# Kernel tuning notes

Measured on AMD Instinct MI355X. Metric: run time of the kernel, lower is better.

The kernel has to match this reference:

```python
import jax, jax.numpy as jnp
import numpy as np


def setup_inputs() -> dict:
    key = jax.random.key(0)
    ks = jax.random.split(key, 7)
    N, C, sy, sx = 1024, 384, 7, 7
    Dm, Dc = 64, 64
    Dg = C + Dm + Dc  # 512, must match f_t_global
    return {
        "f_t_global": jax.random.normal(ks[0], (N, Dg), dtype=jnp.float32),
        "x_t_local": jax.random.normal(ks[1], (N, C, sy, sx), dtype=jnp.float32),
        "x_t_prev_local": jax.random.normal(ks[2], (N, C, sy, sx), dtype=jnp.float32),
        "m_t": jax.random.normal(ks[3], (N, Dm), dtype=jnp.float32),
        "m_t_prev": jax.random.normal(ks[4], (N, Dm), dtype=jnp.float32),
        "c_t": jax.random.normal(ks[5], (N, Dc), dtype=jnp.float32),
        "c_t_prev": jax.random.normal(ks[6], (N, Dc), dtype=jnp.float32),
    }


def _join(loc, m, c):
    # loc: [S, N, C]; m: [N, Dm]; c: [N, Dc] -> [S, N, C+Dm+Dc]
    S, N, _ = loc.shape
    mc = jnp.concatenate([m, c], axis=-1)  # [N, Dm+Dc]
    mc = jnp.broadcast_to(mc[None], (S, N, mc.shape[-1]))
    return jnp.concatenate([loc, mc], axis=-1)


def _mean_ce_diag(logits):
    # logits: [S, N, N]; labels = arange(N) for every s -> mean over s of CE
    logp = jax.nn.log_softmax(logits, axis=-1)
    diag = jnp.diagonal(logp, axis1=1, axis2=2)  # [S, N]
    return -jnp.mean(diag)  # mean over N (per-step CE) and over S (the /(sx*sy))


def reference(f_t_global, x_t_local, x_t_prev_local, m_t, m_t_prev, c_t, c_t_prev):
    N, C, sy, sx = x_t_prev_local.shape
    S = sy * sx
    # [N,C,sy,sx] -> [S,N,C] (spatial locations batched)
    prev = x_t_prev_local.reshape(N, C, S).transpose(2, 0, 1)
    cur = x_t_local.reshape(N, C, S).transpose(2, 0, 1)
    pos = _join(prev, m_t_prev, c_t_prev)   # [S, N, D]
    # loss1: global features vs per-location previous positives
    logits1 = jnp.einsum('id,sjd->sij', f_t_global, pos)  # [S, N, N]
    loss1 = _mean_ce_diag(logits1)
    # loss2: per-location current predictions vs previous positives
    pred2 = _join(cur, m_t, c_t)            # [S, N, D]
    logits2 = jnp.einsum('sid,sjd->sij', pred2, pos)
    loss2 = _mean_ce_diag(logits2)
    loss = loss1 + loss2
    return (loss, x_t_prev_local, x_t_local)
```

## Files before the change

kernel.cpp:

```cpp
#include <hip/hip_runtime.h>
#include <hip/hip_bf16.h>

typedef __attribute__((ext_vector_type(8))) __bf16 bf16x8;
typedef __attribute__((ext_vector_type(4))) float  f32x4;

#define SDIM 49
#define NDIM 1024
#define CDIM 384
#define DDIM 512
#define DMC  64
#define SCALE (1.0f/(SDIM*NDIM))
#define SLOT 65536
#define CHUNK 24576

__device__ __forceinline__ void gload16(const void* g, void* l) {
    __builtin_amdgcn_global_load_lds((const __attribute__((address_space(1))) void*)g,
                                     (__attribute__((address_space(3))) void*)l, 16, 0, 0);
}

__global__ __launch_bounds__(512) void pack_kernel(
    const float* __restrict__ xloc, const float* __restrict__ mv,
    const float* __restrict__ cv,   __hip_bfloat16* __restrict__ dst)
{
    const int j = blockIdx.x;
    const int d = threadIdx.x;
    float vals[SDIM];
    if (d < CDIM) {
        const float* p = xloc + ((size_t)j * CDIM + d) * SDIM;
        #pragma unroll
        for (int s = 0; s < SDIM; ++s) vals[s] = p[s];
    } else if (d < CDIM + DMC) {
        float v = mv[j * DMC + (d - CDIM)];
        #pragma unroll
        for (int s = 0; s < SDIM; ++s) vals[s] = v;
    } else {
        float v = cv[j * DMC + (d - CDIM - DMC)];
        #pragma unroll
        for (int s = 0; s < SDIM; ++s) vals[s] = v;
    }
    #pragma unroll
    for (int s = 0; s < SDIM; ++s)
        dst[((size_t)s * NDIM + j) * DDIM + d] = __float2bfloat16(vals[s]);
}

__global__ void fpack_kernel(const float* __restrict__ f,
                             __hip_bfloat16* __restrict__ dst, int n,
                             float* __restrict__ out0)
{
    int i = blockIdx.x * blockDim.x + threadIdx.x;
    if (i == 0) out0[0] = 0.0f;
    if (i < n) dst[i] = __float2bfloat16(f[i]);
}

__global__ __launch_bounds__(512, 2) void loss_kernel(
    const __hip_bfloat16* __restrict__ Fm,
    const __hip_bfloat16* __restrict__ Km,
    const __hip_bfloat16* __restrict__ Qm,
    const float* __restrict__ xp,
    const float* __restrict__ xq,
    float* __restrict__ outv,
    float2* __restrict__ part,
    float* __restrict__ out)
{
    extern __shared__ __attribute__((aligned(16))) char sm[];

    const int bid = blockIdx.x;
    const int xcd = bid & 7;
    const int jj  = bid >> 3;
    const int g0  = 196 * xcd;
    const int gend = g0 + 196;

    const int tid  = threadIdx.x;
    const int lane = tid & 63;
    const int w    = tid >> 6;
    const int l15  = lane & 15;
    const int l4   = lane >> 4;
    const int wk   = w >> 2;
    const int wq   = w & 3;

    const int trow = tid >> 3;
    const int scol = (((tid & 7) ^ ((tid >> 3) & 7)) << 4);

    const unsigned xo   = (unsigned)((l15 & 7) << 4);
    const unsigned arow = (unsigned)((wk * 128 + l15) * 128);
    const unsigned brow = 32768u + (unsigned)((wq * 64 + l15) * 128);

    auto APtr = [&](int g) -> const char* {
        const int s = g >> 5, kb = (g >> 3) & 3;
        return (const char*)Km + ((size_t)s * NDIM + (size_t)kb * 256) * 1024;
    };
    auto BPtr = [&](int g) -> const char* {
        const int s = g >> 5, qb = g & 7;
        return (qb < 4)
            ? ((const char*)Fm + (size_t)qb * 256 * 1024)
            : ((const char*)Qm + ((size_t)s * NDIM + (size_t)(qb - 4) * 256) * 1024);
    };
    auto stage8 = [&](const char* A, const char* B, int ko, char* slot) {
        #pragma unroll
        for (int c = 0; c < 4; ++c) {
            gload16(A + (size_t)(c * 64 + trow) * 1024 + ko + scol,
                    slot + c * 8192 + tid * 16);
            gload16(B + (size_t)(c * 64 + trow) * 1024 + ko + scol,
                    slot + 32768 + c * 8192 + tid * 16);
        }
    };

    f32x4 acc[8][4];
    bf16x8 afr[8], bfr[4];

    #define READ12(KC) do {                                                   \
        const unsigned co = ((unsigned)((KC) * 64 + l4 * 16)) ^ xo;           \
        _Pragma("unroll")                                                     \
        for (int a = 0; a < 8; ++a)                                           \
            afr[a] = *(const bf16x8*)(sb_ + arow + a * 2048u + co);           \
        _Pragma("unroll")                                                     \
        for (int b = 0; b < 4; ++b)                                           \
            bfr[b] = *(const bf16x8*)(sb_ + brow + b * 2048u + co);           \
    } while (0)

    #define MFMA32() do {                                                     \
        _Pragma("unroll")                                                     \
        for (int a = 0; a < 8; ++a)                                           \
            _Pragma("unroll")                                                 \
            for (int b = 0; b < 4; ++b)                                       \
                acc[a][b] = __builtin_amdgcn_mfma_f32_16x16x32_bf16(          \
                    afr[a], bfr[b], acc[a][b], 0, 0, 0);                      \
    } while (0)

    stage8(APtr(g0 + jj), BPtr(g0 + jj), 0, sm);

    for (int g = g0 + jj; g < gend; g += 32) {
        const char* Ag = APtr(g);
        const char* Bg = BPtr(g);
        const bool hasNext = (g + 32) < gend;
        const char* An = hasNext ? APtr(g + 32) : Ag;
        const char* Bn = hasNext ? BPtr(g + 32) : Bg;

        #pragma unroll
        for (int a = 0; a < 8; ++a)
            #pragma unroll
            for (int b = 0; b < 4; ++b) acc[a][b] = f32x4{0.f, 0.f, 0.f, 0.f};

        #pragma unroll
        for (int t = 0; t < 8; ++t) {
            const char* sb_ = sm + (size_t)(t & 1) * SLOT;
            char* ns_ = sm + (size_t)((t + 1) & 1) * SLOT;

            __syncthreads();

            if ((t < 7) || hasNext) {
                const char* sA = (t < 7) ? Ag : An;
                const char* sB = (t < 7) ? Bg : Bn;
                stage8(sA, sB, (t < 7) ? (t + 1) * 128 : 0, ns_);
            }
            __builtin_amdgcn_sched_barrier(0);

            READ12(0);
            __builtin_amdgcn_s_setprio(1); MFMA32(); __builtin_amdgcn_s_setprio(0);
            READ12(1);
            __builtin_amdgcn_s_setprio(1); MFMA32(); __builtin_amdgcn_s_setprio(0);
        }

        const int s  = g >> 5;
        const int kb = (g >> 3) & 3;
        const int qb = g & 7;

        const float* csrc = (g < 784) ? (xp + (size_t)g * CHUNK)
                                      : (xq + (size_t)(g - 784) * CHUNK);
        float* cdst = outv + (size_t)g * CHUNK;
        f32x4 cbuf[12];
        #pragma unroll
        for (int i = 0; i < 12; ++i)
            cbuf[i] = *(const f32x4*)(csrc + tid * 4 + i * 2048);

        float q_m[4], q_s[4];
        #pragma unroll
        for (int b = 0; b < 4; ++b) {
            float m = -3.0e38f;
            #pragma unroll
            for (int a = 0; a < 8; ++a)
                #pragma unroll
                for (int r = 0; r < 4; ++r) m = fmaxf(m, acc[a][b][r]);
            float ss = 0.0f;
            #pragma unroll
            for (int a = 0; a < 8; ++a)
                #pragma unroll
                for (int r = 0; r < 4; ++r) ss += __expf(acc[a][b][r] - m);
            #pragma unroll
            for (int off = 16; off <= 32; off <<= 1) {
                float mo = __shfl_xor(m, off, 64);
                float so = __shfl_xor(ss, off, 64);
                float nm = fmaxf(m, mo);
                ss = ss * __expf(m - nm) + so * __expf(mo - nm);
                m = nm;
            }
            q_m[b] = m; q_s[b] = ss;
        }

        if (kb == (qb & 3) && (wq >> 1) == wk) {
            float d = 0.0f;
            const bool lok = (((lane >> 2) & 3) == l4);
            if (wq & 1) {
                #pragma unroll
                for (int b = 0; b < 4; ++b)
                    #pragma unroll
                    for (int r = 0; r < 4; ++r)
                        if (lok && r == (lane & 3)) d += acc[4 + b][b][r];
            } else {
                #pragma unroll
                for (int b = 0; b < 4; ++b)
                    #pragma unroll
                    for (int r = 0; r < 4; ++r)
                        if (lok && r == (lane & 3)) d += acc[b][b][r];
            }
            #pragma unroll
            for (int off = 1; off < 64; off <<= 1) d += __shfl_xor(d, off, 64);
            if (lane == 0) atomicAdd(out, -d * SCALE);
        }

        #pragma unroll
        for (int i = 0; i < 12; ++i)
            *(f32x4*)(cdst + tid * 4 + i * 2048) = cbuf[i];

        if (lane < 16) {
            const size_t rowb = (size_t)s * 2048 + (size_t)qb * 256 + wq * 64 + lane;
            #pragma unroll
            for (int b = 0; b < 4; ++b)
                part[(rowb + b * 16) * 8 + kb * 2 + wk] = make_float2(q_m[b], q_s[b]);
        }
    }
    #undef READ12
    #undef MFMA32
}

__global__ __launch_bounds__(256) void reduce_kernel(
    const float2* __restrict__ part, float* __restrict__ out)
{
    const int row = blockIdx.x * 256 + threadIdx.x;
    const float2* p = part + (size_t)row * 8;
    float m = -3.0e38f;
    float2 q[8];
    #pragma unroll
    for (int i = 0; i < 8; ++i) { q[i] = p[i]; m = fmaxf(m, q[i].x); }
    float ssum = 0.0f;
    #pragma unroll
    for (int i = 0; i < 8; ++i) ssum += q[i].y * __expf(q[i].x - m);
    float v = m + __logf(ssum);
    #pragma unroll
    for (int off = 1; off < 64; off <<= 1) v += __shfl_xor(v, off, 64);
    __shared__ float red[4];
    const int lane = threadIdx.x & 63, w = threadIdx.x >> 6;
    if (lane == 0) red[w] = v;
    __syncthreads();
    if (threadIdx.x == 0)
        atomicAdd(out, (red[0] + red[1] + red[2] + red[3]) * SCALE);
}

extern "C" void kernel_launch(void* const* d_in, const int* in_sizes, int n_in,
                              void* d_out, int out_size, void* d_ws, size_t ws_size,
                              hipStream_t stream)
{
    (void)in_sizes; (void)n_in; (void)out_size; (void)ws_size;
    const float* f  = (const float*)d_in[0];
    const float* x  = (const float*)d_in[1];
    const float* xp = (const float*)d_in[2];
    const float* mt = (const float*)d_in[3];
    const float* mp = (const float*)d_in[4];
    const float* ct = (const float*)d_in[5];
    const float* cp = (const float*)d_in[6];
    float* out = (float*)d_out;

    char* ws = (char*)d_ws;
    const size_t packBytes = (size_t)SDIM * NDIM * DDIM * 2;
    __hip_bfloat16* Km = (__hip_bfloat16*)ws;
    __hip_bfloat16* Qm = (__hip_bfloat16*)(ws + packBytes);
    __hip_bfloat16* Fm = (__hip_bfloat16*)(ws + 2 * packBytes);
    float2* part = (float2*)(ws + 2 * packBytes + (size_t)NDIM * DDIM * 2);

    pack_kernel<<<NDIM, 512, 0, stream>>>(xp, mp, cp, Km);
    pack_kernel<<<NDIM, 512, 0, stream>>>(x,  mt, ct, Qm);
    fpack_kernel<<<(NDIM * DDIM + 255) / 256, 256, 0, stream>>>(f, Fm, NDIM * DDIM, out);

    loss_kernel<<<256, 512, 2 * SLOT, stream>>>(Fm, Km, Qm, xp, x, out + 1, part, out);
    reduce_kernel<<<392, 256, 0, stream>>>(part, out);
}
```

Before: 221.1 us.

## Replace double-buffered 128-wide K stages with 4-slot 64-wide pipeline and vmcnt waits

The GEMM main loop moves from two 64KB LDS slots holding 128-element K chunks to four 32KB slots holding 64-element chunks, prefetching three stages ahead. The full __syncthreads is replaced by s_waitcnt vmcnt counts plus a raw s_barrier, so global loads stay in flight across iterations. The LDS swizzle changes from an XOR pattern to a rotation suited to the 64-byte rows. Total LDS stays the same, but barrier count doubles and the hand-tuned vmcnt counts must match exactly how many loads each stage issues, which is fragile.

```diff
diff --git a/kernel.cpp b/kernel.cpp
--- a/kernel.cpp
+++ b/kernel.cpp
@@ -10,7 +10,7 @@
 #define DDIM 512
 #define DMC  64
 #define SCALE (1.0f/(SDIM*NDIM))
-#define SLOT 65536
+#define SLOT4 32768
 #define CHUNK 24576
 
 __device__ __forceinline__ void gload16(const void* g, void* l) {
@@ -78,12 +78,12 @@
     const int wk   = w >> 2;
     const int wq   = w & 3;
 
-    const int trow = tid >> 3;
-    const int scol = (((tid & 7) ^ ((tid >> 3) & 7)) << 4);
-
-    const unsigned xo   = (unsigned)((l15 & 7) << 4);
-    const unsigned arow = (unsigned)((wk * 128 + l15) * 128);
-    const unsigned brow = 32768u + (unsigned)((wq * 64 + l15) * 128);
+    const int srow = tid >> 2;
+    const int jcol = (((tid & 3) - ((tid >> 3) & 3)) & 3) << 4;
+
+    const unsigned off   = (unsigned)(((l4 + (l15 >> 1)) & 3) << 4);
+    const unsigned abase = (unsigned)((wk * 128 + l15) * 64);
+    const unsigned bbase = 16384u + (unsigned)((wq * 64 + l15) * 64);
 
     auto APtr = [&](int g) -> const char* {
         const int s = g >> 5, kb = (g >> 3) & 3;
@@ -95,27 +95,26 @@
             ? ((const char*)Fm + (size_t)qb * 256 * 1024)
             : ((const char*)Qm + ((size_t)s * NDIM + (size_t)(qb - 4) * 256) * 1024);
     };
-    auto stage8 = [&](const char* A, const char* B, int ko, char* slot) {
-        #pragma unroll
-        for (int c = 0; c < 4; ++c) {
-            gload16(A + (size_t)(c * 64 + trow) * 1024 + ko + scol,
+    auto stage4 = [&](const char* A, const char* B, int ko, char* slot) {
+        #pragma unroll
+        for (int c = 0; c < 2; ++c) {
+            gload16(A + (size_t)(c * 128 + srow) * 1024 + ko + jcol,
                     slot + c * 8192 + tid * 16);
-            gload16(B + (size_t)(c * 64 + trow) * 1024 + ko + scol,
-                    slot + 32768 + c * 8192 + tid * 16);
+            gload16(B + (size_t)(c * 128 + srow) * 1024 + ko + jcol,
+                    slot + 16384 + c * 8192 + tid * 16);
         }
     };
 
     f32x4 acc[8][4];
     bf16x8 afr[8], bfr[4];
 
-    #define READ12(KC) do {                                                   \
-        const unsigned co = ((unsigned)((KC) * 64 + l4 * 16)) ^ xo;           \
+    #define READ12() do {                                                     \
         _Pragma("unroll")                                                     \
         for (int a = 0; a < 8; ++a)                                           \
-            afr[a] = *(const bf16x8*)(sb_ + arow + a * 2048u + co);           \
+            afr[a] = *(const bf16x8*)(sb_ + abase + a * 1024u + off);         \
         _Pragma("unroll")                                                     \
         for (int b = 0; b < 4; ++b)                                           \
-            bfr[b] = *(const bf16x8*)(sb_ + brow + b * 2048u + co);           \
+            bfr[b] = *(const bf16x8*)(sb_ + bbase + b * 1024u + off);         \
     } while (0)
 
     #define MFMA32() do {                                                     \
@@ -127,7 +126,14 @@
                     afr[a], bfr[b], acc[a][b], 0, 0, 0);                      \
     } while (0)
 
-    stage8(APtr(g0 + jj), BPtr(g0 + jj), 0, sm);
+    {
+        const char* A0 = APtr(g0 + jj);
+        const char* B0 = BPtr(g0 + jj);
+        stage4(A0, B0, 0,   sm);
+        stage4(A0, B0, 64,  sm + SLOT4);
+        stage4(A0, B0, 128, sm + 2 * SLOT4);
+        asm volatile("s_waitcnt vmcnt(0)" ::: "memory");
+    }
 
     for (int g = g0 + jj; g < gend; g += 32) {
         const char* Ag = APtr(g);
@@ -142,22 +148,23 @@
             for (int b = 0; b < 4; ++b) acc[a][b] = f32x4{0.f, 0.f, 0.f, 0.f};
 
         #pragma unroll
-        for (int t = 0; t < 8; ++t) {
-            const char* sb_ = sm + (size_t)(t & 1) * SLOT;
-            char* ns_ = sm + (size_t)((t + 1) & 1) * SLOT;
-
-            __syncthreads();
-
-            if ((t < 7) || hasNext) {
-                const char* sA = (t < 7) ? Ag : An;
-                const char* sB = (t < 7) ? Bg : Bn;
-                stage8(sA, sB, (t < 7) ? (t + 1) * 128 : 0, ns_);
+        for (int t = 0; t < 16; ++t) {
+            const char* sb_ = sm + (size_t)(t & 3) * SLOT4;
+            char* ns_ = sm + (size_t)((t + 3) & 3) * SLOT4;
+
+            if (t == 15)      asm volatile("s_waitcnt vmcnt(0)" ::: "memory");
+            else if (t == 14) asm volatile("s_waitcnt vmcnt(4)" ::: "memory");
+            else if (t >= 3)  asm volatile("s_waitcnt vmcnt(8)" ::: "memory");
+            __builtin_amdgcn_s_barrier();
+
+            if (t <= 12) {
+                stage4(Ag, Bg, (t + 3) * 64, ns_);
+            } else if (hasNext) {
+                stage4(An, Bn, (t - 13) * 64, ns_);
             }
             __builtin_amdgcn_sched_barrier(0);
 
-            READ12(0);
-            __builtin_amdgcn_s_setprio(1); MFMA32(); __builtin_amdgcn_s_setprio(0);
-            READ12(1);
+            READ12();
             __builtin_amdgcn_s_setprio(1); MFMA32(); __builtin_amdgcn_s_setprio(0);
         }
 
@@ -187,9 +194,9 @@
                 #pragma unroll
                 for (int r = 0; r < 4; ++r) ss += __expf(acc[a][b][r] - m);
             #pragma unroll
-            for (int off = 16; off <= 32; off <<= 1) {
-                float mo = __shfl_xor(m, off, 64);
-                float so = __shfl_xor(ss, off, 64);
+            for (int off2 = 16; off2 <= 32; off2 <<= 1) {
+                float mo = __shfl_xor(m, off2, 64);
+                float so = __shfl_xor(ss, off2, 64);
                 float nm = fmaxf(m, mo);
                 ss = ss * __expf(m - nm) + so * __expf(mo - nm);
                 m = nm;
@@ -214,10 +221,11 @@
                         if (lok && r == (lane & 3)) d += acc[b][b][r];
             }
             #pragma unroll
-            for (int off = 1; off < 64; off <<= 1) d += __shfl_xor(d, off, 64);
+            for (int off2 = 1; off2 < 64; off2 <<= 1) d += __shfl_xor(d, off2, 64);
             if (lane == 0) atomicAdd(out, -d * SCALE);
         }
 
+        asm volatile("s_waitcnt vmcnt(0)" ::: "memory");
         #pragma unroll
         for (int i = 0; i < 12; ++i)
             *(f32x4*)(cdst + tid * 4 + i * 2048) = cbuf[i];
@@ -281,6 +289,6 @@
     pack_kernel<<<NDIM, 512, 0, stream>>>(x,  mt, ct, Qm);
     fpack_kernel<<<(NDIM * DDIM + 255) / 256, 256, 0, stream>>>(f, Fm, NDIM * DDIM, out);
 
-    loss_kernel<<<256, 512, 2 * SLOT, stream>>>(Fm, Km, Qm, xp, x, out + 1, part, out);
+    loss_kernel<<<256, 512, 4 * SLOT4, stream>>>(Fm, Km, Qm, xp, x, out + 1, part, out);
     reduce_kernel<<<392, 256, 0, stream>>>(part, out);
 }
```

After: 216.0 us. 1.02x faster.
